# Optimization experiments

Hardware: AMD Instinct MI355X
Metric: run time of the kernel (lower is better)

The kernel has to match this reference:

```python
import jax, jax.numpy as jnp
import numpy as np
import math

B, S, H = 8, 1024, 1024
NUM_LABELS = 2

# torch nn.Linear weight [out,in]; we store transposed [in,out] so y = x @ W + b

def _mha(x, mask, qw, qb, kw, kb, vw, vb, ow, ob, n_heads):
    b, s, h = x.shape
    d = h // n_heads
    Q = (x @ qw + qb).reshape(b, s, n_heads, d)
    K = (x @ kw + kb).reshape(b, s, n_heads, d)
    V = (x @ vw + vb).reshape(b, s, n_heads, d)
    scores = jnp.einsum('bqhd,bkhd->bhqk', Q, K) / math.sqrt(d)  # [b,h,s,s]
    if mask is not None:
        scores = jnp.where(mask[:, None, None, :] == 0, jnp.asarray(-1e9, scores.dtype), scores)
    w = jax.nn.softmax(scores, axis=-1)  # dropout is identity in eval mode
    ctx = jnp.einsum('bhqk,bkhd->bqhd', w, V).reshape(b, s, h)
    return ctx @ ow + ob, w


def _linear_params(key, fin, fout):
    k1, k2 = jax.random.split(key)
    lim = 1.0 / math.sqrt(fin)
    w = jax.random.uniform(k1, (fin, fout), jnp.float32, -lim, lim)
    b = jax.random.uniform(k2, (fout,), jnp.float32, -lim, lim)
    return w, b


def setup_inputs() -> dict:
    key = jax.random.key(0)
    ks = jax.random.split(key, 20)
    inp = {
        'hidden_states': jax.random.normal(ks[0], (B, S, H), jnp.float32),
        'attention_mask': jax.random.randint(ks[1], (B, S), 0, 2, jnp.int32),
    }
    i = 2
    for pre in ('beh', 'tmp', 'pat'):
        for nm in ('q', 'k', 'v', 'o'):
            w, b = _linear_params(ks[i], H, H)
            inp[f'{pre}_{nm}w'] = w
            inp[f'{pre}_{nm}b'] = b
            i += 1
    inp['fus1_w'], inp['fus1_b'] = _linear_params(ks[i], 3 * H, H); i += 1
    inp['fus2_w'], inp['fus2_b'] = _linear_params(ks[i], H, H // 2); i += 1
    inp['cls_w'], inp['cls_b'] = _linear_params(ks[i], H // 2, NUM_LABELS)
    return inp


def reference(hidden_states, attention_mask,
              beh_qw, beh_qb, beh_kw, beh_kb, beh_vw, beh_vb, beh_ow, beh_ob,
              tmp_qw, tmp_qb, tmp_kw, tmp_kb, tmp_vw, tmp_vb, tmp_ow, tmp_ob,
              pat_qw, pat_qb, pat_kw, pat_kb, pat_vw, pat_vb, pat_ow, pat_ob,
              fus1_w, fus1_b, fus2_w, fus2_b, cls_w, cls_b):
    beh_out, _ = _mha(hidden_states, attention_mask, beh_qw, beh_qb, beh_kw, beh_kb, beh_vw, beh_vb, beh_ow, beh_ob, 8)
    tmp_out, _ = _mha(hidden_states, attention_mask, tmp_qw, tmp_qb, tmp_kw, tmp_kb, tmp_vw, tmp_vb, tmp_ow, tmp_ob, 4)
    pat_out, _ = _mha(hidden_states, attention_mask, pat_qw, pat_qb, pat_kw, pat_kb, pat_vw, pat_vb, pat_ow, pat_ob, 4)
    m = attention_mask[:, :, None].astype(hidden_states.dtype)  # [B,S,1]
    denom = m.sum(axis=1)  # [B,1] broadcast like torch expand_as sum
    beh_p = (beh_out * m).sum(axis=1) / denom
    tmp_p = (tmp_out * m).sum(axis=1) / denom
    pat_p = (pat_out * m).sum(axis=1) / denom
    fused = jnp.concatenate([beh_p, tmp_p, pat_p], axis=-1)  # [B,3H]
    h1 = jax.nn.relu(fused @ fus1_w + fus1_b)
    h2 = jax.nn.relu(h1 @ fus2_w + fus2_b)
    logits = h2 @ cls_w + cls_b
    return logits
```

## Files before the change

kernel.cpp:

```cpp
#include <hip/hip_runtime.h>

#define DEVINL __device__ __forceinline__
typedef __attribute__((ext_vector_type(8))) __bf16 bf16x8;
typedef __attribute__((ext_vector_type(4))) __bf16 bf16x4;
typedef __attribute__((ext_vector_type(4))) float f32x4;

DEVINL void gload16(void* lds, const void* g) {
  __builtin_amdgcn_global_load_lds((const __attribute__((address_space(1))) void*)g,
                                   (__attribute__((address_space(3))) void*)lds, 16, 0, 0);
}

__global__ void cvt_bf16_kernel(const float* __restrict__ in, __bf16* __restrict__ out, int n4) {
  int i = blockIdx.x * 256 + threadIdx.x;
  if (i >= n4) return;
  float4 v = reinterpret_cast<const float4*>(in)[i];
  bf16x4 o;
  o.x = (__bf16)v.x; o.y = (__bf16)v.y; o.z = (__bf16)v.z; o.w = (__bf16)v.w;
  reinterpret_cast<bf16x4*>(out)[i] = o;
}

__global__ void wt_pack_kernel(const float* __restrict__ Wq, const float* __restrict__ Wk,
                               const float* __restrict__ Wv, __bf16* __restrict__ WT) {
  __shared__ float t[64][65];
  int k0 = blockIdx.x * 64;
  int n0 = blockIdx.y * 64;
  const float* W = (n0 < 1024) ? Wq : (n0 < 2048 ? Wk : Wv);
  int nn0 = n0 & 1023;
  int r = threadIdx.x >> 6, c = threadIdx.x & 63;
#pragma unroll
  for (int i = 0; i < 16; ++i)
    t[r + i*4][c] = W[(size_t)(k0 + r + i*4) * 1024 + nn0 + c];
  __syncthreads();
#pragma unroll
  for (int i = 0; i < 16; ++i) {
    int row = r + i*4;
    WT[(size_t)(n0 + row) * 1024 + k0 + c] = (__bf16)t[c][row];
  }
}

__global__ __launch_bounds__(256) void gemm_qkv_kernel(
    const __bf16* __restrict__ A, const __bf16* __restrict__ WT,
    const float* __restrict__ bq, const float* __restrict__ bk, const float* __restrict__ bv,
    __bf16* __restrict__ C) {
  constexpr int N_ = 3072, K_ = 1024;
  __shared__ __align__(16) __bf16 lds[2][(128 + 128) * 64];
  int tid = threadIdx.x;
  int lane = tid & 63;
  int wave = tid >> 6;
  int l15 = lane & 15, l4 = lane >> 4;
  int wr = wave >> 1, wc = wave & 1;
  int n0 = blockIdx.x * 128, m0 = blockIdx.y * 128;

  f32x4 acc[4][4] = {};

  const char* Abase = (const char*)(A  + (size_t)m0 * K_);
  const char* Bbase = (const char*)(WT + (size_t)n0 * K_);

  auto STAGE = [&](int buf, int kt) {
    char* Al = (char*)lds[buf];
    char* Bl = (char*)(lds[buf] + 128 * 64);
#pragma unroll
    for (int i = 0; i < 4; ++i) {
      int c = i * 256 + tid;
      int r = c >> 3, cc = c & 7, g = cc ^ (r & 7);
      gload16(Al + (size_t)(c & ~63) * 16,
              Abase + (size_t)r * (K_ * 2) + kt * 128 + g * 16);
      gload16(Bl + (size_t)(c & ~63) * 16,
              Bbase + (size_t)r * (K_ * 2) + kt * 128 + g * 16);
    }
  };

  int cur = 0;
  STAGE(0, 0);
  for (int kt = 0; kt < 16; ++kt) {
    if (kt < 15) {
      STAGE(cur ^ 1, kt + 1);
      asm volatile("s_waitcnt vmcnt(8)" ::: "memory");
    } else {
      asm volatile("s_waitcnt vmcnt(0)" ::: "memory");
    }
    __builtin_amdgcn_s_barrier();
    const char* Al = (const char*)lds[cur];
    const char* Bl = (const char*)(lds[cur] + 128 * 64);
#pragma unroll
    for (int kk = 0; kk < 2; ++kk) {
      bf16x8 af[4], bfr[4];
      int j = kk * 4 + l4;
#pragma unroll
      for (int m = 0; m < 4; ++m) {
        int row = wr * 64 + m * 16 + l15;
        af[m] = *(const bf16x8*)(Al + ((size_t)row * 8 + (j ^ (row & 7))) * 16);
      }
#pragma unroll
      for (int n = 0; n < 4; ++n) {
        int row = wc * 64 + n * 16 + l15;
        bfr[n] = *(const bf16x8*)(Bl + ((size_t)row * 8 + (j ^ (row & 7))) * 16);
      }
      __builtin_amdgcn_s_setprio(1);
#pragma unroll
      for (int m = 0; m < 4; ++m)
#pragma unroll
        for (int n = 0; n < 4; ++n)
          acc[m][n] = __builtin_amdgcn_mfma_f32_16x16x32_bf16(af[m], bfr[n], acc[m][n], 0, 0, 0);
      __builtin_amdgcn_s_setprio(0);
    }
    __builtin_amdgcn_s_barrier();
    cur ^= 1;
  }

#pragma unroll
  for (int n = 0; n < 4; ++n) {
    int col = n0 + wc * 64 + n * 16 + l15;
    const float* bias = (col < 1024) ? bq : (col < 2048 ? bk : bv);
    float bv_ = bias[col & 1023];
#pragma unroll
    for (int m = 0; m < 4; ++m) {
      int rowb = m0 + wr * 64 + m * 16 + l4 * 4;
#pragma unroll
      for (int r = 0; r < 4; ++r)
        C[(size_t)(rowb + r) * N_ + col] = (__bf16)(acc[m][n][r] + bv_);
    }
  }
}

__global__ void vt_pack_kernel(const __bf16* __restrict__ QKV, __bf16* __restrict__ Vt,
                               int hcnt, int D) {
  __shared__ __bf16 t[64][65];
  int s0 = blockIdx.x * 64, d0 = blockIdx.y * 64;
  int bh = blockIdx.z;
  int b = bh / hcnt, h = bh - b*hcnt;
  int r = threadIdx.x >> 6, c = threadIdx.x & 63;
  const __bf16* src = QKV + (size_t)b*1024*3072 + 2048 + (size_t)h*D;
#pragma unroll
  for (int i = 0; i < 16; ++i)
    t[r + i*4][c] = src[(size_t)(s0 + r + i*4)*3072 + d0 + c];
  __syncthreads();
  __bf16* dst = Vt + ((size_t)bh*D + d0)*1024 + s0;
#pragma unroll
  for (int i = 0; i < 16; ++i) {
    int row = r + i*4;
    dst[(size_t)row*1024 + c] = t[c][row];
  }
}

template<int D, int WQ, int HCNT>
__global__ __launch_bounds__(256) void attn_kernel(
    const __bf16* __restrict__ QKV, const __bf16* __restrict__ Vt,
    const int* __restrict__ mask, float* __restrict__ ctx) {
  constexpr int QT  = 4*WQ;
  constexpr int QB  = 1024/QT;
  constexpr int MT  = WQ/16;
  constexpr int KC  = D/32;
  constexpr int NT2 = D/16;
  constexpr int CPR = D/8;
  __shared__ __align__(16) __bf16 smem[64*D + D*64 + 4*WQ*72];
  __bf16* Kl = smem;
  __bf16* Vl = smem + 64*D;
  __bf16* Pl = smem + 128*D;

  int tid = threadIdx.x;
  int lane = tid & 63, wave = tid >> 6;
  int l15 = lane & 15, l4 = lane >> 4;
  int d = blockIdx.x;
  int xcd = d & 7, j = d >> 3;
  int qb = j % QB, g = j / QB;
  int p = g*8 + xcd;
  int h = p % HCNT, b = p / HCNT;
  int q0 = qb * QT;
  const float scale = (D == 128) ? 0.08838834764831845f : 0.0625f;

  {
    const char* qbase = (const char*)(QKV + (size_t)(b*1024 + q0)*3072 + (size_t)h*D);
    for (int c0 = 0; c0 < QT*D/8; c0 += 256) {
      int c = c0 + tid;
      int row = c / CPR, cc = c % CPR;
      gload16((char*)smem + (c0 + (tid & ~63))*16,
              qbase + (size_t)row*6144 + ((cc ^ (row & 7))*16));
    }
  }
  __syncthreads();
  bf16x8 qf[MT][KC];
#pragma unroll
  for (int m = 0; m < MT; ++m)
#pragma unroll
    for (int kc = 0; kc < KC; ++kc) {
      int row = wave*WQ + m*16 + l15;
      int boff = ((kc*32 + l4*8)*2) ^ ((row & 7) << 4);
      qf[m][kc] = *(const bf16x8*)((const char*)smem + (size_t)row*(D*2) + boff);
    }
  __syncthreads();

  f32x4 ao[MT][NT2] = {};
  float dsum[MT][4] = {};

  const char* kbase = (const char*)(QKV + (size_t)(b*1024)*3072 + 1024 + (size_t)h*D);
  const char* vbase = (const char*)(Vt + (size_t)(b*HCNT + h)*D*1024);

  auto STAGE_K = [&](int t) {
    for (int c0 = 0; c0 < 8*D; c0 += 256) {
      int c = c0 + tid;
      int row = c / CPR, cc = c % CPR;
      gload16((char*)Kl + (c0 + (tid & ~63))*16,
              kbase + (size_t)(t*64 + row)*6144 + ((cc ^ (row & 7))*16));
    }
  };
  auto STAGE_V = [&](int t) {
    for (int c0 = 0; c0 < 8*D; c0 += 256) {
      int c = c0 + tid;
      int row = c >> 3, cc = c & 7;
      gload16((char*)Vl + (c0 + (tid & ~63))*16,
              vbase + (size_t)row*2048 + t*128 + ((cc ^ (row & 7))*16));
    }
  };

  STAGE_K(0);
  for (int t = 0; t < 16; ++t) {
    __syncthreads();
    STAGE_V(t);
    float mv[4];
#pragma unroll
    for (int n = 0; n < 4; ++n)
      mv[n] = (float)mask[b*1024 + t*64 + n*16 + l15];

#pragma unroll
    for (int n = 0; n < 4; ++n) {
      f32x4 s[MT] = {};
#pragma unroll
      for (int kc = 0; kc < KC; ++kc) {
        int krow = n*16 + l15;
        int boff = ((kc*32 + l4*8)*2) ^ ((krow & 7) << 4);
        bf16x8 kf = *(const bf16x8*)((const char*)Kl + (size_t)krow*(D*2) + boff);
#pragma unroll
        for (int m = 0; m < MT; ++m)
          s[m] = __builtin_amdgcn_mfma_f32_16x16x32_bf16(qf[m][kc], kf, s[m], 0, 0, 0);
      }
#pragma unroll
      for (int m = 0; m < MT; ++m)
#pragma unroll
        for (int r = 0; r < 4; ++r) {
          float pf_ = __expf(s[m][r] * scale) * mv[n];
          __bf16 pb = (__bf16)pf_;
          dsum[m][r] += (float)pb;
          Pl[(size_t)(wave*WQ + m*16 + l4*4 + r)*72 + n*16 + l15] = pb;
        }
    }
    __syncthreads();
    if (t < 15) STAGE_K(t + 1);

    bf16x8 pfr[MT][2];
#pragma unroll
    for (int m = 0; m < MT; ++m)
#pragma unroll
      for (int kk = 0; kk < 2; ++kk)
        pfr[m][kk] = *(const bf16x8*)(Pl + (size_t)(wave*WQ + m*16 + l15)*72 + kk*32 + l4*8);
#pragma unroll
    for (int n2 = 0; n2 < NT2; ++n2) {
      bf16x8 vf[2];
#pragma unroll
      for (int kk = 0; kk < 2; ++kk) {
        int vrow = n2*16 + l15;
        int boff = ((kk*32 + l4*8)*2) ^ ((vrow & 7) << 4);
        vf[kk] = *(const bf16x8*)((const char*)Vl + (size_t)vrow*128 + boff);
      }
#pragma unroll
      for (int m = 0; m < MT; ++m)
#pragma unroll
        for (int kk = 0; kk < 2; ++kk)
          ao[m][n2] = __builtin_amdgcn_mfma_f32_16x16x32_bf16(pfr[m][kk], vf[kk], ao[m][n2], 0, 0, 0);
    }
  }

  float inv[MT][4];
#pragma unroll
  for (int m = 0; m < MT; ++m)
#pragma unroll
    for (int r = 0; r < 4; ++r) {
      float v = dsum[m][r];
      v += __shfl_xor(v, 1, 64);
      v += __shfl_xor(v, 2, 64);
      v += __shfl_xor(v, 4, 64);
      v += __shfl_xor(v, 8, 64);
      inv[m][r] = 1.0f / v;
    }
#pragma unroll
  for (int m = 0; m < MT; ++m) {
    int rowb = b*1024 + q0 + wave*WQ + m*16 + l4*4;
#pragma unroll
    for (int n2 = 0; n2 < NT2; ++n2) {
      int col = h*D + n2*16 + l15;
#pragma unroll
      for (int r = 0; r < 4; ++r)
        ctx[(size_t)(rowb + r)*1024 + col] = ao[m][n2][r] * inv[m][r];
    }
  }
}

__global__ void denom_kernel(const int* __restrict__ mask, float* __restrict__ denom) {
  int b = blockIdx.x, t = threadIdx.x;
  int acc = 0;
  for (int s = t; s < 1024; s += 256) acc += mask[b*1024 + s];
  for (int o = 32; o; o >>= 1) acc += __shfl_down(acc, o, 64);
  __shared__ int red[4];
  if ((t & 63) == 0) red[t >> 6] = acc;
  __syncthreads();
  if (t == 0) denom[b] = (float)(red[0] + red[1] + red[2] + red[3]);
}

__global__ void pool_partial_kernel(const float* __restrict__ ctx, const int* __restrict__ mask,
                                    float* __restrict__ part) {
  int sc = blockIdx.x;
  int b  = blockIdx.y;
  int t  = threadIdx.x;
  const float* base = ctx + (size_t)b*1024*1024 + (size_t)sc*32*1024;
  const int* mrow = mask + b*1024 + sc*32;
  float4 acc = {0.f, 0.f, 0.f, 0.f};
  for (int s = 0; s < 32; ++s) {
    if (mrow[s]) {
      float4 v = reinterpret_cast<const float4*>(base + (size_t)s*1024)[t];
      acc.x += v.x; acc.y += v.y; acc.z += v.z; acc.w += v.w;
    }
  }
  reinterpret_cast<float4*>(part + ((size_t)b*32 + sc)*1024)[t] = acc;
}

__global__ void pool_reduce_kernel(const float* __restrict__ part, const float* __restrict__ denom,
                                   float* __restrict__ out) {
  int i = blockIdx.x*256 + threadIdx.x;
  int b = i >> 10, c = i & 1023;
  float a = 0.f;
#pragma unroll
  for (int sc = 0; sc < 32; ++sc) a += part[((size_t)b*32 + sc)*1024 + c];
  out[i] = a / denom[b];
}

__global__ void oproj_partial_kernel(const float* __restrict__ pooled,
    const float* __restrict__ W0, const float* __restrict__ W1, const float* __restrict__ W2,
    float* __restrict__ part) {
  int ai = blockIdx.z;
  const float* W = (ai == 0) ? W0 : (ai == 1 ? W1 : W2);
  int ks = blockIdx.y, k0 = ks*128;
  __shared__ float xl[8*128];
  const float* P = pooled + ai*8192;
  for (int i = threadIdx.x; i < 8*128; i += 256) {
    int b = i >> 7, kk = i & 127;
    xl[i] = P[b*1024 + k0 + kk];
  }
  __syncthreads();
  int n = blockIdx.x*256 + threadIdx.x;
  float acc[8] = {};
  for (int kk = 0; kk < 128; ++kk) {
    float w = W[(size_t)(k0+kk)*1024 + n];
#pragma unroll
    for (int b = 0; b < 8; ++b) acc[b] += xl[b*128 + kk] * w;
  }
#pragma unroll
  for (int b = 0; b < 8; ++b) part[(((size_t)ai*8 + ks)*8 + b)*1024 + n] = acc[b];
}

__global__ void oproj_reduce_kernel(const float* __restrict__ part,
    const float* __restrict__ b0, const float* __restrict__ b1, const float* __restrict__ b2,
    float* __restrict__ fused) {
  int i = blockIdx.x*256 + threadIdx.x;
  int ai = i >> 13, rem = i & 8191;
  int b = rem >> 10, n = rem & 1023;
  const float* bb = (ai == 0) ? b0 : (ai == 1 ? b1 : b2);
  float a = bb[n];
#pragma unroll
  for (int ks = 0; ks < 8; ++ks) a += part[(((size_t)ai*8 + ks)*8 + b)*1024 + n];
  fused[b*3072 + ai*1024 + n] = a;
}

__global__ void fc_partial_kernel(const float* __restrict__ X, const float* __restrict__ W,
                                  float* __restrict__ part, int Kin, int Nout, int kchunk) {
  extern __shared__ float xl[];
  int ks = blockIdx.y, k0 = ks*kchunk;
  for (int i = threadIdx.x; i < 8*kchunk; i += 256) {
    int b = i / kchunk, kk = i - b*kchunk;
    xl[i] = X[b*Kin + k0 + kk];
  }
  __syncthreads();
  int n = blockIdx.x*256 + threadIdx.x;
  float acc[8] = {};
  for (int kk = 0; kk < kchunk; ++kk) {
    float w = W[(size_t)(k0+kk)*Nout + n];
#pragma unroll
    for (int b = 0; b < 8; ++b) acc[b] += xl[b*kchunk + kk] * w;
  }
#pragma unroll
  for (int b = 0; b < 8; ++b) part[((size_t)ks*8 + b)*Nout + n] = acc[b];
}

__global__ void fc_reduce_kernel(const float* __restrict__ part, const float* __restrict__ bias,
                                 float* __restrict__ out, int Nout, int KS, int do_relu) {
  int i = blockIdx.x*256 + threadIdx.x;
  int b = i / Nout, n = i - b*Nout;
  float a = bias[n];
  for (int ks = 0; ks < KS; ++ks) a += part[((size_t)ks*8 + b)*Nout + n];
  out[i] = do_relu ? fmaxf(a, 0.f) : a;
}

__global__ void cls_kernel(const float* __restrict__ h2, const float* __restrict__ W,
                           const float* __restrict__ bias, float* __restrict__ out) {
  int t = threadIdx.x;
  int o = t >> 4, sl = t & 15;
  int b = o >> 1, n = o & 1;
  float a = 0.f;
  for (int k = sl; k < 512; k += 16) a += h2[b*512 + k] * W[k*2 + n];
#pragma unroll
  for (int m = 1; m < 16; m <<= 1) a += __shfl_xor(a, m, 64);
  if (sl == 0) out[o] = a + bias[n];
}

extern "C" void kernel_launch(void* const* d_in, const int* in_sizes, int n_in,
                              void* d_out, int out_size, void* d_ws, size_t ws_size,
                              hipStream_t stream) {
  const float* X   = (const float*)d_in[0];
  const int* mask  = (const int*)d_in[1];
  const float* w_[3][8];
  for (int a = 0; a < 3; ++a)
    for (int j = 0; j < 8; ++j)
      w_[a][j] = (const float*)d_in[2 + a*8 + j];
  const float* fus1_w = (const float*)d_in[26];
  const float* fus1_b = (const float*)d_in[27];
  const float* fus2_w = (const float*)d_in[28];
  const float* fus2_b = (const float*)d_in[29];
  const float* cls_w  = (const float*)d_in[30];
  const float* cls_b  = (const float*)d_in[31];

  char* p = (char*)d_ws;
  auto carve = [&](size_t bytes) { char* r = p; p += (bytes + 255) & ~(size_t)255; return r; };
  __bf16* Xb    = (__bf16*)carve((size_t)8192*1024*2);
  __bf16* WTb   = (__bf16*)carve((size_t)3072*1024*2);
  __bf16* QKVb  = (__bf16*)carve((size_t)8192*3072*2);
  __bf16* Vtb   = (__bf16*)carve((size_t)8192*1024*2);
  float* ctxb   = (float*)carve((size_t)8192*1024*4);
  float* pooledb= (float*)carve(3*8*1024*4);
  float* denomb = (float*)carve(256);
  float* fusedb = (float*)carve(8*3072*4);
  float* partb  = (float*)carve((size_t)24*8*1024*4);
  float* opartb = (float*)carve((size_t)3*8*8*1024*4);
  float* poolpartb = (float*)carve((size_t)8*32*1024*4);
  float* h1b    = (float*)carve(8*1024*4);
  float* h2b    = (float*)carve(8*512*4);
  if ((size_t)(p - (char*)d_ws) > ws_size) return;

  cvt_bf16_kernel<<<8192, 256, 0, stream>>>(X, Xb, 8192*1024/4);
  denom_kernel<<<8, 256, 0, stream>>>(mask, denomb);

  for (int a = 0; a < 3; ++a) {
    wt_pack_kernel<<<dim3(16,48), 256, 0, stream>>>(w_[a][0], w_[a][2], w_[a][4], WTb);
    gemm_qkv_kernel<<<dim3(24,64), 256, 0, stream>>>(Xb, WTb, w_[a][1], w_[a][3], w_[a][5], QKVb);
    if (a == 0) {
      vt_pack_kernel<<<dim3(16,2,64), 256, 0, stream>>>(QKVb, Vtb, 8, 128);
      attn_kernel<128,32,8><<<512, 256, 0, stream>>>(QKVb, Vtb, mask, ctxb);
    } else {
      vt_pack_kernel<<<dim3(16,4,32), 256, 0, stream>>>(QKVb, Vtb, 4, 256);
      attn_kernel<256,16,4><<<512, 256, 0, stream>>>(QKVb, Vtb, mask, ctxb);
    }
    pool_partial_kernel<<<dim3(32,8), 256, 0, stream>>>(ctxb, mask, poolpartb);
    pool_reduce_kernel<<<32, 256, 0, stream>>>(poolpartb, denomb, pooledb + a*8192);
  }

  oproj_partial_kernel<<<dim3(4,8,3), 256, 0, stream>>>(pooledb,
      w_[0][6], w_[1][6], w_[2][6], opartb);
  oproj_reduce_kernel<<<96, 256, 0, stream>>>(opartb,
      w_[0][7], w_[1][7], w_[2][7], fusedb);
  fc_partial_kernel<<<dim3(4,24), 256, 8*128*4, stream>>>(fusedb, fus1_w, partb, 3072, 1024, 128);
  fc_reduce_kernel<<<32, 256, 0, stream>>>(partb, fus1_b, h1b, 1024, 24, 1);
  fc_partial_kernel<<<dim3(2,8), 256, 8*128*4, stream>>>(h1b, fus2_w, partb, 1024, 512, 128);
  fc_reduce_kernel<<<16, 256, 0, stream>>>(partb, fus2_b, h2b, 512, 8, 1);
  cls_kernel<<<1, 256, 0, stream>>>(h2b, cls_w, cls_b, (float*)d_out);
}
```

Baseline: 502.7 us.

## Fuse masked mean-pooling into attention epilogue, drop full context buffer

The attention kernel now reduces its output tile over query rows, weighted by the mask, inside the block. It writes one partial sum per query block instead of storing the full fp32 context tensor. This removes a 32 MB write and re-read per attention branch and drops the separate pool_partial kernel. The reduce kernel takes a variable number of query-block partials. The cost is extra shuffles, shared-memory traffic and two barriers in the epilogue.

```diff
diff --git a/kernel.cpp b/kernel.cpp
--- a/kernel.cpp
+++ b/kernel.cpp
@@ -146,7 +146,7 @@
 template<int D, int WQ, int HCNT>
 __global__ __launch_bounds__(256) void attn_kernel(
     const __bf16* __restrict__ QKV, const __bf16* __restrict__ Vt,
-    const int* __restrict__ mask, float* __restrict__ ctx) {
+    const int* __restrict__ mask, float* __restrict__ pp) {
   constexpr int QT  = 4*WQ;
   constexpr int QB  = 1024/QT;
   constexpr int MT  = WQ/16;
@@ -282,16 +282,32 @@
       v += __shfl_xor(v, 8, 64);
       inv[m][r] = 1.0f / v;
     }
-#pragma unroll
-  for (int m = 0; m < MT; ++m) {
-    int rowb = b*1024 + q0 + wave*WQ + m*16 + l4*4;
-#pragma unroll
-    for (int n2 = 0; n2 < NT2; ++n2) {
-      int col = h*D + n2*16 + l15;
+
+  float mrow[MT][4];
+#pragma unroll
+  for (int m = 0; m < MT; ++m)
+#pragma unroll
+    for (int r = 0; r < 4; ++r)
+      mrow[m][r] = (float)mask[b*1024 + q0 + wave*WQ + m*16 + l4*4 + r];
+
+  float* fl = (float*)smem;
+  __syncthreads();
+#pragma unroll
+  for (int n2 = 0; n2 < NT2; ++n2) {
+    float pa = 0.f;
+#pragma unroll
+    for (int m = 0; m < MT; ++m)
 #pragma unroll
       for (int r = 0; r < 4; ++r)
-        ctx[(size_t)(rowb + r)*1024 + col] = ao[m][n2][r] * inv[m][r];
-    }
+        pa += mrow[m][r] * ao[m][n2][r] * inv[m][r];
+    pa += __shfl_xor(pa, 16, 64);
+    pa += __shfl_xor(pa, 32, 64);
+    if (l4 == 0) fl[wave*D + n2*16 + l15] = pa;
+  }
+  __syncthreads();
+  for (int c = tid; c < D; c += 256) {
+    float s_ = fl[c] + fl[D + c] + fl[2*D + c] + fl[3*D + c];
+    pp[((size_t)(b*QB + qb))*1024 + h*D + c] = s_;
   }
 }
 
@@ -306,30 +322,12 @@
   if (t == 0) denom[b] = (float)(red[0] + red[1] + red[2] + red[3]);
 }
 
-__global__ void pool_partial_kernel(const float* __restrict__ ctx, const int* __restrict__ mask,
-                                    float* __restrict__ part) {
-  int sc = blockIdx.x;
-  int b  = blockIdx.y;
-  int t  = threadIdx.x;
-  const float* base = ctx + (size_t)b*1024*1024 + (size_t)sc*32*1024;
-  const int* mrow = mask + b*1024 + sc*32;
-  float4 acc = {0.f, 0.f, 0.f, 0.f};
-  for (int s = 0; s < 32; ++s) {
-    if (mrow[s]) {
-      float4 v = reinterpret_cast<const float4*>(base + (size_t)s*1024)[t];
-      acc.x += v.x; acc.y += v.y; acc.z += v.z; acc.w += v.w;
-    }
-  }
-  reinterpret_cast<float4*>(part + ((size_t)b*32 + sc)*1024)[t] = acc;
-}
-
 __global__ void pool_reduce_kernel(const float* __restrict__ part, const float* __restrict__ denom,
-                                   float* __restrict__ out) {
+                                   float* __restrict__ out, int QB) {
   int i = blockIdx.x*256 + threadIdx.x;
   int b = i >> 10, c = i & 1023;
   float a = 0.f;
-#pragma unroll
-  for (int sc = 0; sc < 32; ++sc) a += part[((size_t)b*32 + sc)*1024 + c];
+  for (int qb = 0; qb < QB; ++qb) a += part[((size_t)(b*QB + qb))*1024 + c];
   out[i] = a / denom[b];
 }
 
@@ -433,13 +431,12 @@
   __bf16* WTb   = (__bf16*)carve((size_t)3072*1024*2);
   __bf16* QKVb  = (__bf16*)carve((size_t)8192*3072*2);
   __bf16* Vtb   = (__bf16*)carve((size_t)8192*1024*2);
-  float* ctxb   = (float*)carve((size_t)8192*1024*4);
   float* pooledb= (float*)carve(3*8*1024*4);
   float* denomb = (float*)carve(256);
   float* fusedb = (float*)carve(8*3072*4);
   float* partb  = (float*)carve((size_t)24*8*1024*4);
   float* opartb = (float*)carve((size_t)3*8*8*1024*4);
-  float* poolpartb = (float*)carve((size_t)8*32*1024*4);
+  float* poolpartb = (float*)carve((size_t)8*16*1024*4);
   float* h1b    = (float*)carve(8*1024*4);
   float* h2b    = (float*)carve(8*512*4);
   if ((size_t)(p - (char*)d_ws) > ws_size) return;
@@ -452,13 +449,13 @@
     gemm_qkv_kernel<<<dim3(24,64), 256, 0, stream>>>(Xb, WTb, w_[a][1], w_[a][3], w_[a][5], QKVb);
     if (a == 0) {
       vt_pack_kernel<<<dim3(16,2,64), 256, 0, stream>>>(QKVb, Vtb, 8, 128);
-      attn_kernel<128,32,8><<<512, 256, 0, stream>>>(QKVb, Vtb, mask, ctxb);
+      attn_kernel<128,32,8><<<512, 256, 0, stream>>>(QKVb, Vtb, mask, poolpartb);
+      pool_reduce_kernel<<<32, 256, 0, stream>>>(poolpartb, denomb, pooledb + a*8192, 8);
     } else {
       vt_pack_kernel<<<dim3(16,4,32), 256, 0, stream>>>(QKVb, Vtb, 4, 256);
-      attn_kernel<256,16,4><<<512, 256, 0, stream>>>(QKVb, Vtb, mask, ctxb);
-    }
-    pool_partial_kernel<<<dim3(32,8), 256, 0, stream>>>(ctxb, mask, poolpartb);
-    pool_reduce_kernel<<<32, 256, 0, stream>>>(poolpartb, denomb, pooledb + a*8192);
+      attn_kernel<256,16,4><<<512, 256, 0, stream>>>(QKVb, Vtb, mask, poolpartb);
+      pool_reduce_kernel<<<32, 256, 0, stream>>>(poolpartb, denomb, pooledb + a*8192, 16);
+    }
   }
 
   oproj_partial_kernel<<<dim3(4,8,3), 256, 0, stream>>>(pooledb,
```

Result: faster. 479.2 us (-4.7%).
